# Optimization experiments

Measured on AMD Instinct MI355X. Metric: run time of the kernel, lower is better.

## Reference

```python
import jax, jax.numpy as jnp
import numpy as np

N = 50000        # nodes
E_RAND = 800000  # random edges (self-loops appended -> E = 850000)
H = 8            # num_heads
D = 32           # h_feat_dim
IN = 128         # in_feat_dim
SM = 256         # sm_dim
SP = 128         # sp_dim
NEG_SLOPE = 0.2  # DGL GATv2Conv default


def setup_inputs() -> dict:
    key = jax.random.key(0)
    ks = jax.random.split(key, 16)
    s = 0.05
    self_loops = jnp.arange(N, dtype=jnp.int32)
    return {
        "sm_feats": jax.random.normal(ks[0], (N, SM), jnp.float32),
        "sp_feats": jax.random.normal(ks[1], (N, SP), jnp.float32),
        "src": jnp.concatenate([jax.random.randint(ks[2], (E_RAND,), 0, N, jnp.int32), self_loops]),
        "dst": jnp.concatenate([jax.random.randint(ks[3], (E_RAND,), 0, N, jnp.int32), self_loops]),
        # T1 / T2 linears
        "T1_w": jax.random.normal(ks[4], (SM, IN), jnp.float32) * s,
        "T1_b": jnp.zeros((IN,), jnp.float32),
        "T2_w": jax.random.normal(ks[5], (SP, IN), jnp.float32) * s,
        "T2_b": jnp.zeros((IN,), jnp.float32),
        # GATv2 layer 1: in = 2*IN
        "g1_src_w": jax.random.normal(ks[6], (2 * IN, H * D), jnp.float32) * s,
        "g1_dst_w": jax.random.normal(ks[7], (2 * IN, H * D), jnp.float32) * s,
        "g1_attn": jax.random.normal(ks[8], (H, D), jnp.float32) * s,
        "g1_bias": jnp.zeros((H * D,), jnp.float32),
        # GATv2 layer 2: in = D (after head-mean)
        "g2_src_w": jax.random.normal(ks[9], (D, H * D), jnp.float32) * s,
        "g2_dst_w": jax.random.normal(ks[10], (D, H * D), jnp.float32) * s,
        "g2_attn": jax.random.normal(ks[11], (H, D), jnp.float32) * s,
        "g2_bias": jnp.zeros((H * D,), jnp.float32),
    }


def gatv2_conv(x, src, dst, w_src, w_dst, attn, bias):
    # DGL GATv2Conv (share_weights=False, bias=True, no residual/activation)
    feat_src = (x @ w_src).reshape(-1, H, D)   # [N,H,D]
    feat_dst = (x @ w_dst).reshape(-1, H, D)   # [N,H,D]
    e = jax.nn.leaky_relu(feat_src[src] + feat_dst[dst], NEG_SLOPE)  # [E,H,D]
    score = jnp.einsum('ehd,hd->eh', e, attn)  # [E,H]
    # edge softmax over incoming edges per destination (self-loops ensure non-empty)
    smax = jax.ops.segment_max(score, dst, num_segments=N)           # [N,H]
    ex = jnp.exp(score - smax[dst])
    denom = jax.ops.segment_sum(ex, dst, num_segments=N)             # [N,H]
    alpha = ex / denom[dst]                                          # [E,H]
    out = jax.ops.segment_sum(alpha[:, :, None] * feat_src[src], dst, num_segments=N)  # [N,H,D]
    return out + bias.reshape(1, H, D)


def reference(sm_feats, sp_feats, src, dst,
              T1_w, T1_b, T2_w, T2_b,
              g1_src_w, g1_dst_w, g1_attn, g1_bias,
              g2_src_w, g2_dst_w, g2_attn, g2_bias):
    in_feat = jnp.concatenate([sm_feats @ T1_w + T1_b,
                               sp_feats @ T2_w + T2_b], axis=1)      # [N, 2*IN]
    h = gatv2_conv(in_feat, src, dst, g1_src_w, g1_dst_w, g1_attn, g1_bias)
    h = jax.nn.elu(h).mean(axis=1)                                   # [N, D]
    h = gatv2_conv(h, src, dst, g2_src_w, g2_dst_w, g2_attn, g2_bias)
    return h.mean(axis=1)                                            # [N, D]
```

## Files before the change

### kernel.cpp

```cpp
#include <hip/hip_runtime.h>
#include <hip/hip_fp16.h>


typedef unsigned int uint32;
typedef unsigned short u16;
typedef short short8 __attribute__((ext_vector_type(8)));
typedef float f32x4 __attribute__((ext_vector_type(4)));
typedef _Float16 f16x2 __attribute__((ext_vector_type(2)));

union H2 { f16x2 v; uint32 u; };

__device__ __forceinline__ uint32 bf_rne(uint32 u) { return (u + 0x7fffu + ((u >> 16) & 1u)) >> 16; }

__device__ __forceinline__ void split_trunc(float a, float b, uint32& h, uint32& l) {
  uint32 ua = __float_as_uint(a), ub = __float_as_uint(b);
  h = __builtin_amdgcn_perm(ub, ua, 0x07060302u);
  float ra = a - __uint_as_float(ua & 0xffff0000u);
  float rb = b - __uint_as_float(ub & 0xffff0000u);
  l = __builtin_amdgcn_perm(__float_as_uint(rb), __float_as_uint(ra), 0x07060302u);
}

__device__ __forceinline__ int wave_incl_scan(int x) {
  int lane = threadIdx.x & 63;
#pragma unroll
  for (int off = 1; off < 64; off <<= 1) {
    int t = __shfl_up(x, off, 64);
    if (lane >= off) x += t;
  }
  return x;
}

__global__ __launch_bounds__(256) void k_deg(const int* __restrict__ dst, int* __restrict__ deg, int E) {
  int e = blockIdx.x * 256 + threadIdx.x;
  if (e < E) atomicAdd(&deg[dst[e]], 1);
}

__global__ __launch_bounds__(256) void k_blkscan(const int* __restrict__ in, int* __restrict__ out,
                                                 int* __restrict__ blksum, int n) {
  __shared__ int wsum[4];
  int tid = threadIdx.x;
  int i0 = blockIdx.x * 1024 + tid * 4;
  int v0 = 0, v1 = 0, v2 = 0, v3 = 0;
  if (i0 + 3 < n) {
    int4 t = *(const int4*)(in + i0);
    v0 = t.x; v1 = t.y; v2 = t.z; v3 = t.w;
  } else {
    if (i0 < n) v0 = in[i0];
    if (i0 + 1 < n) v1 = in[i0 + 1];
    if (i0 + 2 < n) v2 = in[i0 + 2];
    if (i0 + 3 < n) v3 = in[i0 + 3];
  }
  int ts = v0 + v1 + v2 + v3;
  int incl = wave_incl_scan(ts);
  int lane = tid & 63, wid = tid >> 6;
  if (lane == 63) wsum[wid] = incl;
  __syncthreads();
  if (tid == 0) {
    int a = wsum[0], b = wsum[1], c = wsum[2], d = wsum[3];
    wsum[0] = 0; wsum[1] = a; wsum[2] = a + b; wsum[3] = a + b + c;
    blksum[blockIdx.x] = a + b + c + d;
  }
  __syncthreads();
  int excl = wsum[wid] + incl - ts;
  if (i0 + 3 < n) {
    int4 o; o.x = excl; o.y = excl + v0; o.z = excl + v0 + v1; o.w = excl + v0 + v1 + v2;
    *(int4*)(out + i0) = o;
  } else {
    if (i0 < n) out[i0] = excl;
    if (i0 + 1 < n) out[i0 + 1] = excl + v0;
    if (i0 + 2 < n) out[i0 + 2] = excl + v0 + v1;
    if (i0 + 3 < n) out[i0 + 3] = excl + v0 + v1 + v2;
  }
}

__global__ void k_scan_top(int* __restrict__ bs, int G) {
  int lane = threadIdx.x;
  int base = 0;
  for (int s = 0; s < G; s += 64) {
    int i = s + lane;
    int v = (i < G) ? bs[i] : 0;
    int incl = wave_incl_scan(v);
    if (i < G) bs[i] = base + incl - v;
    base += __shfl(incl, 63, 64);
  }
}

__global__ __launch_bounds__(256) void k_addoff(int* __restrict__ rp, const int* __restrict__ bs, int n, int Etot) {
  int i = blockIdx.x * 256 + threadIdx.x;
  if (i < n) rp[i] += bs[i >> 10];
  if (i == 0) rp[n] = Etot;
}

__global__ __launch_bounds__(256) void k_fill(const int* __restrict__ src, const int* __restrict__ dst,
                                              const int* __restrict__ rp, int* __restrict__ cnt,
                                              int* __restrict__ csr_src, int E) {
  int e = blockIdx.x * 256 + threadIdx.x;
  if (e < E) {
    int d = dst[e];
    int p = rp[d] + atomicAdd(&cnt[d], 1);
    csr_src[p] = src[e];
  }
}

__global__ __launch_bounds__(256) void k_precomb(const float* __restrict__ T1w, const float* __restrict__ T1b,
                                                 const float* __restrict__ T2w, const float* __restrict__ T2b,
                                                 const float* __restrict__ G1, const float* __restrict__ G2,
                                                 u16* __restrict__ Bh, u16* __restrict__ Bl,
                                                 float* __restrict__ cvec) {
  int bb = blockIdx.x;
  const float* G = (bb < 385) ? G1 : G2;
  int off = (bb < 385) ? 0 : 256;
  int r = (bb < 385) ? bb : bb - 385;
  int j = threadIdx.x;
  float acc = 0.f;
  if (r < 256) {
    for (int m = 0; m < 128; m++) acc += T1w[r * 128 + m] * G[m * 256 + j];
  } else if (r < 384) {
    int rr = r - 256;
    for (int m = 0; m < 128; m++) acc += T2w[rr * 128 + m] * G[(128 + m) * 256 + j];
  } else {
    for (int m = 0; m < 128; m++) acc += T1b[m] * G[m * 256 + j] + T2b[m] * G[(128 + m) * 256 + j];
    cvec[off + j] = acc;
    return;
  }
  uint32 u = __float_as_uint(acc);
  uint32 hi = bf_rne(u);
  float rest = acc - __uint_as_float(hi << 16);
  uint32 lo = __float_as_uint(rest) >> 16;
  int k = r, colabs = off + j;
  int kt = k >> 5, lq = (k >> 3) & 3, j8 = k & 7;
  int cb = colabs >> 7, colr = colabs & 127, ni = colr >> 4, lr = colr & 15;
  size_t idx = ((size_t)(((cb * 12 + kt) * 8 + ni) * 4 + lq) * 16 + lr) * 8 + j8;
  Bh[idx] = (u16)hi;
  Bl[idx] = (u16)lo;
}

#define GLL(GP, LP)                                                     \
  __builtin_amdgcn_global_load_lds(                                     \
      (const __attribute__((address_space(1))) void*)(GP),              \
      (__attribute__((address_space(3))) void*)(LP), 16, 0, 0)

__global__ __launch_bounds__(256, 4) void k_gemm(const float* __restrict__ sm, const float* __restrict__ sp,
                                                 const u16* __restrict__ Bth, const u16* __restrict__ Btl,
                                                 const float* __restrict__ cvec, __half* __restrict__ fs,
                                                 __half* __restrict__ fd, int N) {
  __shared__ u16 BH[2][4096];
  __shared__ u16 BL[2][4096];
  int tid = threadIdx.x, w = tid >> 6, l = tid & 63;
  int lr = l & 15, lq = l >> 4;
  int L = blockIdx.x;
  int x = L & 7, m = L >> 3;
  int cb = m & 3;
  int rb = x + 8 * (m >> 2);
  int col0 = cb * 128, row0 = rb * 128;
  if (row0 >= N) return;
  int r0 = row0 + w * 32 + lr;
  int r1 = r0 + 16;
  int c0 = r0 < N ? r0 : N - 1;
  int c1 = r1 < N ? r1 : N - 1;
  const float* psm0 = sm + (size_t)c0 * 256 + lq * 8;
  const float* psm1 = sm + (size_t)c1 * 256 + lq * 8;
  const float* psp0 = sp + (size_t)c0 * 128 + lq * 8;
  const float* psp1 = sp + (size_t)c1 * 128 + lq * 8;

  f32x4 acc[2][8];
#pragma unroll
  for (int mt = 0; mt < 2; mt++)
#pragma unroll
    for (int ni = 0; ni < 8; ni++) acc[mt][ni] = (f32x4){0.f, 0.f, 0.f, 0.f};

#define STAGE_B(S, BUF)                                                 \
  {                                                                     \
    size_t g0 = (size_t)(cb * 12 + (S)) * 4096;                         \
    _Pragma("unroll") for (int i = 0; i < 2; i++) {                     \
      int c = i * 256 + tid;                                            \
      int lb = (i * 4 + w) * 512;                                       \
      GLL(Bth + g0 + (size_t)c * 8, &BH[BUF][lb]);                      \
      GLL(Btl + g0 + (size_t)c * 8, &BL[BUF][lb]);                      \
    }                                                                   \
  }

  STAGE_B(0, 0);

#pragma unroll
  for (int st = 0; st < 12; st++) {
    const int cu = st & 1, nx = cu ^ 1;
    __syncthreads();
    const float* ga0 = (st < 8) ? (psm0 + st * 32) : (psp0 + (st - 8) * 32);
    const float* ga1 = (st < 8) ? (psm1 + st * 32) : (psp1 + (st - 8) * 32);
    float4 v00 = *(const float4*)(ga0);
    float4 v01 = *(const float4*)(ga0 + 4);
    float4 v10 = *(const float4*)(ga1);
    float4 v11 = *(const float4*)(ga1 + 4);
    if (st < 11) STAGE_B(st + 1, nx);
    uint4 H0, L0, H1, L1;
    split_trunc(v00.x, v00.y, H0.x, L0.x);
    split_trunc(v00.z, v00.w, H0.y, L0.y);
    split_trunc(v01.x, v01.y, H0.z, L0.z);
    split_trunc(v01.z, v01.w, H0.w, L0.w);
    split_trunc(v10.x, v10.y, H1.x, L1.x);
    split_trunc(v10.z, v10.w, H1.y, L1.y);
    split_trunc(v11.x, v11.y, H1.z, L1.z);
    split_trunc(v11.z, v11.w, H1.w, L1.w);
    short8 a0h = *(short8*)&H0, a0l = *(short8*)&L0;
    short8 a1h = *(short8*)&H1, a1l = *(short8*)&L1;
#pragma unroll
    for (int ni = 0; ni < 8; ni++) {
      int lo = (ni * 64 + l) * 8;
      short8 bh = *(const short8*)&BH[cu][lo];
      short8 bl = *(const short8*)&BL[cu][lo];
      acc[0][ni] = __builtin_amdgcn_mfma_f32_16x16x32_bf16(a0h, bh, acc[0][ni], 0, 0, 0);
      acc[0][ni] = __builtin_amdgcn_mfma_f32_16x16x32_bf16(a0l, bh, acc[0][ni], 0, 0, 0);
      acc[0][ni] = __builtin_amdgcn_mfma_f32_16x16x32_bf16(a0h, bl, acc[0][ni], 0, 0, 0);
      acc[1][ni] = __builtin_amdgcn_mfma_f32_16x16x32_bf16(a1h, bh, acc[1][ni], 0, 0, 0);
      acc[1][ni] = __builtin_amdgcn_mfma_f32_16x16x32_bf16(a1l, bh, acc[1][ni], 0, 0, 0);
      acc[1][ni] = __builtin_amdgcn_mfma_f32_16x16x32_bf16(a1h, bl, acc[1][ni], 0, 0, 0);
    }
  }

#pragma unroll
  for (int mt = 0; mt < 2; mt++) {
    int rbr = row0 + w * 32 + mt * 16 + lq * 4;
#pragma unroll
    for (int ni = 0; ni < 8; ni++) {
      int c = col0 + ni * 16 + lr;
      float cv = cvec[c];
      __half* op = fs; int cc = c;
      if (c >= 256) { op = fd; cc = c - 256; }
#pragma unroll
      for (int r = 0; r < 4; r++) {
        int rr = rbr + r;
        if (rr < N) op[(size_t)rr * 256 + cc] = __float2half(acc[mt][ni][r] + cv);
      }
    }
  }
#undef STAGE_B
}

__global__ __launch_bounds__(256) void k_feat2(const float* __restrict__ h, const float* __restrict__ Ws,
                                               const float* __restrict__ Wd, __half* __restrict__ fs,
                                               __half* __restrict__ fd, int N) {
  int j = threadIdx.x;
  int n0 = blockIdx.x * 32;
  float ws[32], wd[32];
#pragma unroll
  for (int k = 0; k < 32; k++) {
    ws[k] = Ws[k * 256 + j];
    wd[k] = Wd[k * 256 + j];
  }
  int nend = n0 + 32; if (nend > N) nend = N;
#pragma unroll 2
  for (int n = n0; n < nend; n++) {
    const float* hr = h + (size_t)n * 32;
    float as = 0.f, ad = 0.f;
#pragma unroll
    for (int k = 0; k < 32; k++) {
      float hv = hr[k];
      as += hv * ws[k];
      ad += hv * wd[k];
    }
    fs[(size_t)n * 256 + j] = __float2half(as);
    fd[(size_t)n * 256 + j] = __float2half(ad);
  }
}

template <int FINAL>
__global__ __launch_bounds__(256) void k_edge(const uint2* __restrict__ fs, const uint2* __restrict__ fd,
                                              const int* __restrict__ csr_src, const int* __restrict__ rp,
                                              const float* __restrict__ attn, const float* __restrict__ bias,
                                              float* __restrict__ out, int N) {
  int n = blockIdx.x * 4 + (threadIdx.x >> 6);
  if (n >= N) return;
  int lane = threadIdx.x & 63;
  float4 av = ((const float4*)attn)[lane];
  H2 AV01, AV23, Y01, Y23;
  AV01.v = (f16x2){(_Float16)av.x, (_Float16)av.y};
  AV23.v = (f16x2){(_Float16)av.z, (_Float16)av.w};
  const f16x2 c02 = {(_Float16)0.2f, (_Float16)0.2f};
  uint2 yu = fd[(size_t)n * 64 + lane];
  Y01.u = yu.x; Y23.u = yu.y;
  int beg = rp[n], end = rp[n + 1];
  float den0 = 0.f, den1 = 0.f;
  float4 acc0 = {0.f, 0.f, 0.f, 0.f}, acc1 = {0.f, 0.f, 0.f, 0.f};

  auto edge1 = [&](uint2 xu, float& den, float4& acc) {
    H2 Xa, Xb; Xa.u = xu.x; Xb.u = xu.y;
    f16x2 ea = Xa.v + Y01.v, eb = Xb.v + Y23.v;
    f16x2 ta = __builtin_elementwise_max(ea, ea * c02);
    f16x2 tb = __builtin_elementwise_max(eb, eb * c02);
    float p = __builtin_amdgcn_fdot2(ta, AV01.v, 0.f, false);
    p = __builtin_amdgcn_fdot2(tb, AV23.v, p, false);
    p += __shfl_xor(p, 1, 64);
    p += __shfl_xor(p, 2, 64);
    p += __shfl_xor(p, 4, 64);
    float wgt = __expf(p);
    den += wgt;
    acc.x += wgt * (float)Xa.v.x; acc.y += wgt * (float)Xa.v.y;
    acc.z += wgt * (float)Xb.v.x; acc.w += wgt * (float)Xb.v.y;
  };

  int e = beg;
  int nq = (end - beg) >> 2;
  if (nq > 0) {
    int s0 = csr_src[e], s1 = csr_src[e + 1], s2 = csr_src[e + 2], s3 = csr_src[e + 3];
    uint2 x0 = fs[(size_t)s0 * 64 + lane];
    uint2 x1 = fs[(size_t)s1 * 64 + lane];
    uint2 x2 = fs[(size_t)s2 * 64 + lane];
    uint2 x3 = fs[(size_t)s3 * 64 + lane];
    for (int q = 1; q < nq; q++) {
      int b2 = e + 4 * q;
      int t0 = csr_src[b2], t1 = csr_src[b2 + 1], t2 = csr_src[b2 + 2], t3 = csr_src[b2 + 3];
      uint2 y0 = fs[(size_t)t0 * 64 + lane];
      uint2 y1 = fs[(size_t)t1 * 64 + lane];
      uint2 y2 = fs[(size_t)t2 * 64 + lane];
      uint2 y3 = fs[(size_t)t3 * 64 + lane];
      edge1(x0, den0, acc0); edge1(x1, den1, acc1);
      edge1(x2, den0, acc0); edge1(x3, den1, acc1);
      x0 = y0; x1 = y1; x2 = y2; x3 = y3;
    }
    edge1(x0, den0, acc0); edge1(x1, den1, acc1);
    edge1(x2, den0, acc0); edge1(x3, den1, acc1);
    e += 4 * nq;
  }
  for (; e < end; e++) {
    int s0 = csr_src[e];
    uint2 xu = fs[(size_t)s0 * 64 + lane];
    edge1(xu, den0, acc0);
  }

  float4 acc = {acc0.x + acc1.x, acc0.y + acc1.y, acc0.z + acc1.z, acc0.w + acc1.w};
  float invd = 1.f / (den0 + den1);
  float4 b = ((const float4*)bias)[lane];
  acc.x = acc.x * invd + b.x;
  acc.y = acc.y * invd + b.y;
  acc.z = acc.z * invd + b.z;
  acc.w = acc.w * invd + b.w;
  if (!FINAL) {
    acc.x = acc.x > 0.f ? acc.x : expm1f(acc.x);
    acc.y = acc.y > 0.f ? acc.y : expm1f(acc.y);
    acc.z = acc.z > 0.f ? acc.z : expm1f(acc.z);
    acc.w = acc.w > 0.f ? acc.w : expm1f(acc.w);
  }
#pragma unroll
  for (int mask = 8; mask <= 32; mask <<= 1) {
    acc.x += __shfl_xor(acc.x, mask, 64);
    acc.y += __shfl_xor(acc.y, mask, 64);
    acc.z += __shfl_xor(acc.z, mask, 64);
    acc.w += __shfl_xor(acc.w, mask, 64);
  }
  if (lane < 8) {
    float4 o = {acc.x * 0.125f, acc.y * 0.125f, acc.z * 0.125f, acc.w * 0.125f};
    ((float4*)out)[(size_t)n * 8 + lane] = o;
  }
}

extern "C" void kernel_launch(void* const* d_in, const int* in_sizes, int n_in,
                              void* d_out, int out_size, void* d_ws, size_t ws_size,
                              hipStream_t stream) {
  const float* sm  = (const float*)d_in[0];
  const float* sp  = (const float*)d_in[1];
  const int*   src = (const int*)d_in[2];
  const int*   dst = (const int*)d_in[3];
  const float* T1w = (const float*)d_in[4];
  const float* T1b = (const float*)d_in[5];
  const float* T2w = (const float*)d_in[6];
  const float* T2b = (const float*)d_in[7];
  const float* g1sw = (const float*)d_in[8];
  const float* g1dw = (const float*)d_in[9];
  const float* g1a  = (const float*)d_in[10];
  const float* g1b  = (const float*)d_in[11];
  const float* g2sw = (const float*)d_in[12];
  const float* g2dw = (const float*)d_in[13];
  const float* g2a  = (const float*)d_in[14];
  const float* g2b  = (const float*)d_in[15];
  const int N = in_sizes[1] / 128;
  const int E = in_sizes[2];
  float* out = (float*)d_out;

  size_t off = 0;
  char* wsb = (char*)d_ws;
  auto alloc = [&](size_t bytes) -> void* {
    void* p = wsb + off;
    off += (bytes + 255) & ~(size_t)255;
    return p;
  };
  u16* Bth = (u16*)alloc((size_t)512 * 384 * 2);
  u16* Btl = (u16*)alloc((size_t)512 * 384 * 2);
  float* cvec  = (float*)alloc(512 * 4);
  int* deg     = (int*)alloc((size_t)N * 4);
  int* cnt     = (int*)alloc((size_t)N * 4);
  int* row_ptr = (int*)alloc((size_t)(N + 1) * 4);
  int* blksum  = (int*)alloc(4096 * 4);
  int* csr_src = (int*)alloc((size_t)E * 4);
  __half* fs   = (__half*)alloc((size_t)N * 256 * 2);
  __half* fd   = (__half*)alloc((size_t)N * 256 * 2);
  float* hmid  = (float*)alloc((size_t)N * 32 * 4);
  (void)ws_size; (void)n_in; (void)out_size;

  (void)hipMemsetAsync(deg, 0, (size_t)N * 4, stream);
  (void)hipMemsetAsync(cnt, 0, (size_t)N * 4, stream);

  k_deg<<<(E + 255) / 256, 256, 0, stream>>>(dst, deg, E);
  int nblk = (N + 1023) / 1024;
  k_blkscan<<<nblk, 256, 0, stream>>>(deg, row_ptr, blksum, N);
  k_scan_top<<<1, 64, 0, stream>>>(blksum, nblk);
  k_addoff<<<(N + 255) / 256, 256, 0, stream>>>(row_ptr, blksum, N, E);
  k_fill<<<(E + 255) / 256, 256, 0, stream>>>(src, dst, row_ptr, cnt, csr_src, E);

  k_precomb<<<770, 256, 0, stream>>>(T1w, T1b, T2w, T2b, g1sw, g1dw, Bth, Btl, cvec);

  int rbs = (N + 127) / 128;
  int rbp = (rbs + 7) & ~7;
  k_gemm<<<dim3(rbp * 4), 256, 0, stream>>>(sm, sp, Bth, Btl, cvec, fs, fd, N);
  k_edge<0><<<(N + 3) / 4, 256, 0, stream>>>((const uint2*)fs, (const uint2*)fd, csr_src, row_ptr, g1a, g1b, hmid, N);

  k_feat2<<<(N + 31) / 32, 256, 0, stream>>>(hmid, g2sw, g2dw, fs, fd, N);
  k_edge<1><<<(N + 3) / 4, 256, 0, stream>>>((const uint2*)fs, (const uint2*)fd, csr_src, row_ptr, g2a, g2b, out, N);
}
```

Before: 476.6 us.

## Replace split-bf16 triple MFMA GEMM with single fp16 MFMA and triple-buffered pipeline

The input-feature GEMM previously emulated fp32 by splitting A and B into bf16 hi/lo parts and issuing three bf16 MFMAs per tile. It now converts both operands to fp16 and issues one fp16 MFMA, which cuts matrix work to a third and halves B staging traffic. The B tile pipeline becomes three LDS buffers with two stages in flight, A operands are prefetched one step ahead in registers, and explicit vmcnt waits plus barriers replace __syncthreads. The cost is lower precision: fp16 keeps fewer mantissa bits than the old split scheme and can overflow for large values.

```diff
diff --git a/kernel.cpp b/kernel.cpp
--- a/kernel.cpp
+++ b/kernel.cpp
@@ -4,21 +4,11 @@
 
 typedef unsigned int uint32;
 typedef unsigned short u16;
-typedef short short8 __attribute__((ext_vector_type(8)));
 typedef float f32x4 __attribute__((ext_vector_type(4)));
 typedef _Float16 f16x2 __attribute__((ext_vector_type(2)));
+typedef _Float16 f16x8 __attribute__((ext_vector_type(8)));
 
 union H2 { f16x2 v; uint32 u; };
-
-__device__ __forceinline__ uint32 bf_rne(uint32 u) { return (u + 0x7fffu + ((u >> 16) & 1u)) >> 16; }
-
-__device__ __forceinline__ void split_trunc(float a, float b, uint32& h, uint32& l) {
-  uint32 ua = __float_as_uint(a), ub = __float_as_uint(b);
-  h = __builtin_amdgcn_perm(ub, ua, 0x07060302u);
-  float ra = a - __uint_as_float(ua & 0xffff0000u);
-  float rb = b - __uint_as_float(ub & 0xffff0000u);
-  l = __builtin_amdgcn_perm(__float_as_uint(rb), __float_as_uint(ra), 0x07060302u);
-}
 
 __device__ __forceinline__ int wave_incl_scan(int x) {
   int lane = threadIdx.x & 63;
@@ -105,8 +95,7 @@
 __global__ __launch_bounds__(256) void k_precomb(const float* __restrict__ T1w, const float* __restrict__ T1b,
                                                  const float* __restrict__ T2w, const float* __restrict__ T2b,
                                                  const float* __restrict__ G1, const float* __restrict__ G2,
-                                                 u16* __restrict__ Bh, u16* __restrict__ Bl,
-                                                 float* __restrict__ cvec) {
+                                                 __half* __restrict__ Bf, float* __restrict__ cvec) {
   int bb = blockIdx.x;
   const float* G = (bb < 385) ? G1 : G2;
   int off = (bb < 385) ? 0 : 256;
@@ -123,16 +112,11 @@
     cvec[off + j] = acc;
     return;
   }
-  uint32 u = __float_as_uint(acc);
-  uint32 hi = bf_rne(u);
-  float rest = acc - __uint_as_float(hi << 16);
-  uint32 lo = __float_as_uint(rest) >> 16;
   int k = r, colabs = off + j;
   int kt = k >> 5, lq = (k >> 3) & 3, j8 = k & 7;
   int cb = colabs >> 7, colr = colabs & 127, ni = colr >> 4, lr = colr & 15;
   size_t idx = ((size_t)(((cb * 12 + kt) * 8 + ni) * 4 + lq) * 16 + lr) * 8 + j8;
-  Bh[idx] = (u16)hi;
-  Bl[idx] = (u16)lo;
+  Bf[idx] = __float2half(acc);
 }
 
 #define GLL(GP, LP)                                                     \
@@ -141,11 +125,9 @@
       (__attribute__((address_space(3))) void*)(LP), 16, 0, 0)
 
 __global__ __launch_bounds__(256, 4) void k_gemm(const float* __restrict__ sm, const float* __restrict__ sp,
-                                                 const u16* __restrict__ Bth, const u16* __restrict__ Btl,
-                                                 const float* __restrict__ cvec, __half* __restrict__ fs,
-                                                 __half* __restrict__ fd, int N) {
-  __shared__ u16 BH[2][4096];
-  __shared__ u16 BL[2][4096];
+                                                 const u16* __restrict__ Bf, const float* __restrict__ cvec,
+                                                 __half* __restrict__ fs, __half* __restrict__ fd, int N) {
+  __shared__ u16 BFl[3 * 4096];
   int tid = threadIdx.x, w = tid >> 6, l = tid & 63;
   int lr = l & 15, lq = l >> 4;
   int L = blockIdx.x;
@@ -174,47 +156,60 @@
     size_t g0 = (size_t)(cb * 12 + (S)) * 4096;                         \
     _Pragma("unroll") for (int i = 0; i < 2; i++) {                     \
       int c = i * 256 + tid;                                            \
-      int lb = (i * 4 + w) * 512;                                       \
-      GLL(Bth + g0 + (size_t)c * 8, &BH[BUF][lb]);                      \
-      GLL(Btl + g0 + (size_t)c * 8, &BL[BUF][lb]);                      \
+      int lb = (BUF)*4096 + (i * 4 + w) * 512;                          \
+      GLL(Bf + g0 + (size_t)c * 8, &BFl[lb]);                           \
     }                                                                   \
   }
 
+#define LOADA(P, D)                                                     \
+  {                                                                     \
+    const float* _g0 = ((P) < 8) ? (psm0 + (P)*32) : (psp0 + ((P)-8) * 32); \
+    const float* _g1 = ((P) < 8) ? (psm1 + (P)*32) : (psp1 + ((P)-8) * 32); \
+    D[0] = *(const float4*)_g0;                                         \
+    D[1] = *(const float4*)(_g0 + 4);                                   \
+    D[2] = *(const float4*)_g1;                                         \
+    D[3] = *(const float4*)(_g1 + 4);                                   \
+  }
+
+  float4 Aa[4], Ab[4];
+  LOADA(0, Aa);
   STAGE_B(0, 0);
+  STAGE_B(1, 1);
+  asm volatile("s_waitcnt vmcnt(2)" ::: "memory");
+  __builtin_amdgcn_sched_barrier(0);
+  __builtin_amdgcn_s_barrier();
 
 #pragma unroll
   for (int st = 0; st < 12; st++) {
-    const int cu = st & 1, nx = cu ^ 1;
-    __syncthreads();
-    const float* ga0 = (st < 8) ? (psm0 + st * 32) : (psp0 + (st - 8) * 32);
-    const float* ga1 = (st < 8) ? (psm1 + st * 32) : (psp1 + (st - 8) * 32);
-    float4 v00 = *(const float4*)(ga0);
-    float4 v01 = *(const float4*)(ga0 + 4);
-    float4 v10 = *(const float4*)(ga1);
-    float4 v11 = *(const float4*)(ga1 + 4);
-    if (st < 11) STAGE_B(st + 1, nx);
-    uint4 H0, L0, H1, L1;
-    split_trunc(v00.x, v00.y, H0.x, L0.x);
-    split_trunc(v00.z, v00.w, H0.y, L0.y);
-    split_trunc(v01.x, v01.y, H0.z, L0.z);
-    split_trunc(v01.z, v01.w, H0.w, L0.w);
-    split_trunc(v10.x, v10.y, H1.x, L1.x);
-    split_trunc(v10.z, v10.w, H1.y, L1.y);
-    split_trunc(v11.x, v11.y, H1.z, L1.z);
-    split_trunc(v11.z, v11.w, H1.w, L1.w);
-    short8 a0h = *(short8*)&H0, a0l = *(short8*)&L0;
-    short8 a1h = *(short8*)&H1, a1l = *(short8*)&L1;
+    const int slot = st % 3;
+    const float4* Dc = (st & 1) ? Ab : Aa;
+    float4* Dn = (st & 1) ? Aa : Ab;
+    if (st < 11) LOADA(st + 1, Dn);
+    if (st < 10) STAGE_B(st + 2, (st + 2) % 3);
+    f16x8 a0, a1;
+    a0[0] = (_Float16)Dc[0].x; a0[1] = (_Float16)Dc[0].y;
+    a0[2] = (_Float16)Dc[0].z; a0[3] = (_Float16)Dc[0].w;
+    a0[4] = (_Float16)Dc[1].x; a0[5] = (_Float16)Dc[1].y;
+    a0[6] = (_Float16)Dc[1].z; a0[7] = (_Float16)Dc[1].w;
+    a1[0] = (_Float16)Dc[2].x; a1[1] = (_Float16)Dc[2].y;
+    a1[2] = (_Float16)Dc[2].z; a1[3] = (_Float16)Dc[2].w;
+    a1[4] = (_Float16)Dc[3].x; a1[5] = (_Float16)Dc[3].y;
+    a1[6] = (_Float16)Dc[3].z; a1[7] = (_Float16)Dc[3].w;
 #pragma unroll
     for (int ni = 0; ni < 8; ni++) {
-      int lo = (ni * 64 + l) * 8;
-      short8 bh = *(const short8*)&BH[cu][lo];
-      short8 bl = *(const short8*)&BL[cu][lo];
-      acc[0][ni] = __builtin_amdgcn_mfma_f32_16x16x32_bf16(a0h, bh, acc[0][ni], 0, 0, 0);
-      acc[0][ni] = __builtin_amdgcn_mfma_f32_16x16x32_bf16(a0l, bh, acc[0][ni], 0, 0, 0);
-      acc[0][ni] = __builtin_amdgcn_mfma_f32_16x16x32_bf16(a0h, bl, acc[0][ni], 0, 0, 0);
-      acc[1][ni] = __builtin_amdgcn_mfma_f32_16x16x32_bf16(a1h, bh, acc[1][ni], 0, 0, 0);
-      acc[1][ni] = __builtin_amdgcn_mfma_f32_16x16x32_bf16(a1l, bh, acc[1][ni], 0, 0, 0);
-      acc[1][ni] = __builtin_amdgcn_mfma_f32_16x16x32_bf16(a1h, bl, acc[1][ni], 0, 0, 0);
+      int lo = slot * 4096 + (ni * 64 + l) * 8;
+      f16x8 bf = *(const f16x8*)&BFl[lo];
+      acc[0][ni] = __builtin_amdgcn_mfma_f32_16x16x32_f16(a0, bf, acc[0][ni], 0, 0, 0);
+      acc[1][ni] = __builtin_amdgcn_mfma_f32_16x16x32_f16(a1, bf, acc[1][ni], 0, 0, 0);
+    }
+    if (st < 10) {
+      asm volatile("s_waitcnt vmcnt(6)" ::: "memory");
+    } else if (st == 10) {
+      asm volatile("s_waitcnt vmcnt(4)" ::: "memory");
+    }
+    if (st < 11) {
+      __builtin_amdgcn_sched_barrier(0);
+      __builtin_amdgcn_s_barrier();
     }
   }
 
@@ -235,6 +230,7 @@
     }
   }
 #undef STAGE_B
+#undef LOADA
 }
 
 __global__ __launch_bounds__(256) void k_feat2(const float* __restrict__ h, const float* __restrict__ Ws,
@@ -384,8 +380,7 @@
     off += (bytes + 255) & ~(size_t)255;
     return p;
   };
-  u16* Bth = (u16*)alloc((size_t)512 * 384 * 2);
-  u16* Btl = (u16*)alloc((size_t)512 * 384 * 2);
+  __half* Bf  = (__half*)alloc((size_t)512 * 384 * 2);
   float* cvec  = (float*)alloc(512 * 4);
   int* deg     = (int*)alloc((size_t)N * 4);
   int* cnt     = (int*)alloc((size_t)N * 4);
@@ -407,11 +402,11 @@
   k_addoff<<<(N + 255) / 256, 256, 0, stream>>>(row_ptr, blksum, N, E);
   k_fill<<<(E + 255) / 256, 256, 0, stream>>>(src, dst, row_ptr, cnt, csr_src, E);
 
-  k_precomb<<<770, 256, 0, stream>>>(T1w, T1b, T2w, T2b, g1sw, g1dw, Bth, Btl, cvec);
+  k_precomb<<<770, 256, 0, stream>>>(T1w, T1b, T2w, T2b, g1sw, g1dw, Bf, cvec);
 
   int rbs = (N + 127) / 128;
   int rbp = (rbs + 7) & ~7;
-  k_gemm<<<dim3(rbp * 4), 256, 0, stream>>>(sm, sp, Bth, Btl, cvec, fs, fd, N);
+  k_gemm<<<dim3(rbp * 4), 256, 0, stream>>>(sm, sp, (const u16*)Bf, cvec, fs, fd, N);
   k_edge<0><<<(N + 3) / 4, 256, 0, stream>>>((const uint2*)fs, (const uint2*)fd, csr_src, row_ptr, g1a, g1b, hmid, N);
 
   k_feat2<<<(N + 31) / 32, 256, 0, stream>>>(hmid, g2sw, g2dw, fs, fd, N);
```

Result: faster. 462.0 us (-3.1%).
